# Performance work log

Measured on AMD Instinct MI355X. Metric: run time of the kernel, lower is better.

## Reference

```python
import jax, jax.numpy as jnp
import numpy as np


def _conv3x3(x, w, b):
    # stride 1, padding 1, NCHW / OIHW
    y = jax.lax.conv_general_dilated(x, w, (1, 1), ((1, 1), (1, 1)),
                                     dimension_numbers=('NCHW', 'OIHW', 'NCHW'))
    return y + b[None, :, None, None]


def _bilinear(img, py, px):
    """Bilinear sample img [B,C,H,W] at float positions py,px [B,H,W].
    Out-of-bounds corners contribute zero (zero padding), matching DCNv2."""
    B, C, H, W = img.shape
    y0f = jnp.floor(py)
    x0f = jnp.floor(px)
    wy = (py - y0f)[:, None]  # [B,1,H,W]
    wx = (px - x0f)[:, None]
    y0 = y0f.astype(jnp.int32)
    x0 = x0f.astype(jnp.int32)
    flat = img.reshape(B, C, H * W)

    def g(iy, ix):
        valid = ((iy >= 0) & (iy < H) & (ix >= 0) & (ix < W))
        lin = (jnp.clip(iy, 0, H - 1) * W + jnp.clip(ix, 0, W - 1)).reshape(B, 1, -1)
        idx = jnp.broadcast_to(lin, (B, C, lin.shape[-1]))
        v = jnp.take_along_axis(flat, idx, axis=2).reshape(B, C, *iy.shape[1:])
        return v * valid[:, None].astype(img.dtype)

    v00 = g(y0, x0)
    v01 = g(y0, x0 + 1)
    v10 = g(y0 + 1, x0)
    v11 = g(y0 + 1, x0 + 1)
    return (v00 * (1 - wy) * (1 - wx) + v01 * (1 - wy) * wx
            + v10 * wy * (1 - wx) + v11 * wy * wx)


def _dcn(x, ow, ob, w, b):
    """Modulated deformable conv (DCNv2), 3x3, stride 1, pad 1, dg=1."""
    B, C, H, W = x.shape
    om = _conv3x3(x, ow, ob)                       # [B,27,H,W]
    o1, o2, m = jnp.split(om, 3, axis=1)
    off = jnp.concatenate([o1, o2], axis=1)        # [B,18,H,W]
    mask = jax.nn.sigmoid(m)                       # [B,9,H,W]
    oy = off[:, 0::2]                              # [B,9,H,W] y-offset per tap
    ox = off[:, 1::2]                              # [B,9,H,W] x-offset per tap
    ys = jnp.arange(H, dtype=x.dtype)[None, :, None]
    xs = jnp.arange(W, dtype=x.dtype)[None, None, :]
    acc = jnp.zeros((B, w.shape[0], H, W), x.dtype)
    for k in range(9):  # fixed small kernel-tap loop
        ky, kx = divmod(k, 3)
        py = ys + (ky - 1) + oy[:, k]
        px = xs + (kx - 1) + ox[:, k]
        v = _bilinear(x, py, px) * mask[:, k][:, None]   # [B,C,H,W]
        acc = acc + jnp.einsum('bchw,oc->bohw', v, w[:, :, ky, kx])
    return acc + b[None, :, None, None]


def setup_inputs() -> dict:
    key = jax.random.key(0)
    ks = jax.random.split(key, 8)
    B, H, W = 4, 96, 96
    x = jax.random.normal(ks[0], (B, 64, H, W), jnp.float32)

    def offw(k, cin):
        return jax.random.normal(k, (27, cin, 3, 3), jnp.float32) * 0.01

    def mainw(k, cout, cin):
        return jax.random.normal(k, (cout, cin, 3, 3), jnp.float32) * (1.0 / np.sqrt(cin * 9))

    return {
        'x': x,
        'ow1': offw(ks[1], 64), 'ob1': jnp.zeros((27,), jnp.float32),
        'w1': mainw(ks[2], 64, 64), 'b1': jnp.zeros((64,), jnp.float32),
        'ow2': offw(ks[3], 64), 'ob2': jnp.zeros((27,), jnp.float32),
        'w2': mainw(ks[4], 512, 64), 'b2': jnp.zeros((512,), jnp.float32),
        'ow3': offw(ks[5], 512), 'ob3': jnp.zeros((27,), jnp.float32),
        'w3': mainw(ks[6], 256, 512), 'b3': jnp.zeros((256,), jnp.float32),
    }


def reference(x, ow1, ob1, w1, b1, ow2, ob2, w2, b2, ow3, ob3, w3, b3):
    y = _dcn(x, ow1, ob1, w1, b1)
    y = _dcn(y, ow2, ob2, w2, b2)
    y = _dcn(y, ow3, ob3, w3, b3)
    return y
```

## Files before the change

### kernel.cpp

```cpp
#include <hip/hip_runtime.h>
#include <stdint.h>


#define HH 96
#define WW 96
#define BBATCH 4
#define HWP (HH*WW)
#define PTOT (BBATCH*HWP)

typedef _Float16 f16x8 __attribute__((ext_vector_type(8)));
typedef _Float16 h2    __attribute__((ext_vector_type(2)));
typedef float f32x4 __attribute__((ext_vector_type(4)));

union U16x8 { uint4 q; _Float16 h[8]; h2 v[4]; };
union UB    { uint4 q; f16x8 f; };
union UH4   { uint2 d; _Float16 h[4]; };

__global__ void k_nchw2nhwc(const float* __restrict__ in, _Float16* __restrict__ out){
  __shared__ float t[32][33];
  int b = blockIdx.z;
  int p0 = blockIdx.x*32, c0 = blockIdx.y*32;
  int tx = threadIdx.x, ty = threadIdx.y;
  #pragma unroll
  for(int i=0;i<32;i+=8)
    t[ty+i][tx] = in[((size_t)(b*64 + c0+ty+i))*HWP + p0+tx];
  __syncthreads();
  #pragma unroll
  for(int i=0;i<32;i+=8)
    out[((size_t)(b*HWP + p0+ty+i))*64 + c0+tx] = (_Float16)t[tx][ty+i];
}

template<int CIN>
__global__ void k_tow(const float* __restrict__ ow, _Float16* __restrict__ owT){
  int i = blockIdx.x*256 + threadIdx.x;
  if(i >= 9*32*CIN) return;
  int c = i % CIN; int j = (i/CIN)&31; int k = i/(CIN*32);
  owT[i] = (j<27) ? (_Float16)ow[((size_t)(j*CIN + c))*9 + k] : (_Float16)0.f;
}

template<int CIN,int COUT>
__global__ void k_tw(const float* __restrict__ w, _Float16* __restrict__ wTf){
  int i = blockIdx.x*256 + threadIdx.x;
  if(i >= 9*COUT*CIN) return;
  int c = i % CIN; int o = (i/CIN)%COUT; int k = i/(CIN*COUT);
  int g = c>>5, quad = (c>>3)&3, j = c&7;
  int ob = o>>4, l15 = o&15;
  size_t dst = ((((size_t)k*(CIN/32) + g)*(COUT/16) + ob)*64 + quad*16 + l15)*8 + j;
  wTf[dst] = (_Float16)w[((size_t)(o*CIN + c))*9 + k];
}

template<int CIN,int NT>
__launch_bounds__(256,2)
__global__ void k_goffs(const _Float16* __restrict__ xin, const _Float16* __restrict__ owT,
                        float* __restrict__ om){
  __shared__ __align__(16) _Float16 As[64*40];
  __shared__ __align__(16) _Float16 Bs[32*40];
  int pos0 = blockIdx.x*64;
  int K0 = blockIdx.y*NT;
  float* omo = om + (size_t)blockIdx.y*PTOT*32;
  int t = threadIdx.x;
  int lane = t&63, wave = t>>6;
  int quad = lane>>4, l15 = lane&15;
  f32x4 acc[2] = {};
  int pa = t>>2, ca = (t&3)*8;
  int P = pos0 + pa;
  int b = P/HWP, rem = P%HWP;
  int y = rem/WW, x = rem%WW;
  #pragma unroll 1
  for(int k=K0;k<K0+NT;k++){
    int iy = y + k/3 - 1, ix = x + k%3 - 1;
    bool valid = (iy>=0)&&(iy<HH)&&(ix>=0)&&(ix<WW);
    const _Float16* src = xin + (((size_t)b*HWP + iy*WW + ix)*CIN) + ca;
    #pragma unroll 1
    for(int c0=0;c0<CIN;c0+=32){
      uint4 av = make_uint4(0,0,0,0);
      if(valid) av = *(const uint4*)(src + c0);
      *(uint4*)&As[pa*40 + ca] = av;
      if(t < 128){
        int j = t>>2;
        *(uint4*)&Bs[j*40 + ca] = *(const uint4*)(owT + ((size_t)k*32 + j)*CIN + c0 + ca);
      }
      __syncthreads();
      UB afu; afu.q = *(const uint4*)&As[(wave*16 + l15)*40 + quad*8];
      #pragma unroll
      for(int ni=0;ni<2;ni++){
        UB bu; bu.q = *(const uint4*)&Bs[(ni*16 + l15)*40 + quad*8];
        acc[ni] = __builtin_amdgcn_mfma_f32_16x16x32_f16(afu.f, bu.f, acc[ni], 0,0,0);
      }
      __syncthreads();
    }
  }
  #pragma unroll
  for(int ni=0;ni<2;ni++)
    #pragma unroll
    for(int r=0;r<4;r++){
      int row = wave*16 + quad*4 + r;
      omo[(size_t)(pos0+row)*32 + ni*16 + l15] = acc[ni][r];
    }
}

template<int NS>
__global__ void k_prep(const float* __restrict__ om, const float* __restrict__ ob,
                       float* __restrict__ pym){
  int i = blockIdx.x*256 + threadIdx.x;
  if(i >= PTOT*9) return;
  int k = i%9, p = i/9;
  int rem = p%HWP;
  int y = rem/WW, x = rem%WW;
  float oy=0.f, ox=0.f, mm=0.f;
  #pragma unroll
  for(int s=0;s<NS;s++){
    const float* o = om + (size_t)s*PTOT*32 + (size_t)p*32;
    oy += o[2*k]; ox += o[2*k+1]; mm += o[18+k];
  }
  oy += ob[2*k]; ox += ob[2*k+1]; mm += ob[18+k];
  float m = 1.f/(1.f + expf(-mm));
  pym[(size_t)i*3+0] = (float)(y + k/3 - 1) + oy;
  pym[(size_t)i*3+1] = (float)(x + k%3 - 1) + ox;
  pym[(size_t)i*3+2] = m;
}

template<int CIN,int COUT,int BN,int MODE>
__launch_bounds__(256,2)
__global__ void k_gmain(const _Float16* __restrict__ xin, const float* __restrict__ pym,
                        const _Float16* __restrict__ wTf, const float* __restrict__ bias,
                        void* __restrict__ outv){
  constexpr int NW = BN/4;
  constexpr int NF = NW/16;
  constexpr int KG = CIN/32;
  constexpr int OB = COUT/16;
  constexpr int SPT = CIN/64;
  constexpr int NZ = (MODE==1) ? 3 : 1;
  constexpr int KN = (MODE==1) ? 3 : 9;
  constexpr int S = KN*SPT;
  __shared__ __align__(16) _Float16 As[2][64*72];
  int bx = blockIdx.x;
  int q = bx>>3, r = bx&7;
  int z = q - (q/NZ)*NZ;
  int lin = r*((gridDim.x>>3)/NZ) + q/NZ;
  int pos0 = lin*64;
  int o0 = blockIdx.y*BN;
  int K0 = (MODE==1) ? z*3 : 0;
  int t = threadIdx.x;
  int lane = t&63, wave = t>>6;
  int quad = lane>>4, l15 = lane&15;
  f32x4 acc[4][NF] = {};
  int pa = t>>2, ca = (t&3)*16;
  int P = pos0 + pa;
  int b = P/HWP;
  const _Float16* base = xin + (size_t)b*HWP*CIN + ca;
  const uint4* wf = (const uint4*)wTf;
  int obBase = (o0>>4) + wave*NF;

  h2 Wc[4]; int oc_[4];
  h2 Wn[4]; int ocn[4];
  int kc = K0;

  auto tapParams = [&](int k, h2* W, int* oc){
    const float* pp = pym + ((size_t)P*9 + k)*3;
    float py = pp[0], px = pp[1], mk = pp[2];
    float y0f = floorf(py), x0f = floorf(px);
    float wy = py - y0f, wx = px - x0f;
    int iy0 = (int)y0f, ix0 = (int)x0f;
    int iy1 = iy0+1, ix1 = ix0+1;
    bool vy0 = (iy0>=0)&&(iy0<HH), vy1 = (iy1>=0)&&(iy1<HH);
    bool vx0 = (ix0>=0)&&(ix0<WW), vx1 = (ix1>=0)&&(ix1<WW);
    float w00 = (vy0&&vx0) ? (1.f-wy)*(1.f-wx)*mk : 0.f;
    float w01 = (vy0&&vx1) ? (1.f-wy)*wx*mk      : 0.f;
    float w10 = (vy1&&vx0) ? wy*(1.f-wx)*mk      : 0.f;
    float w11 = (vy1&&vx1) ? wy*wx*mk            : 0.f;
    int cy0 = min(max(iy0,0),HH-1), cy1 = min(max(iy1,0),HH-1);
    int cx0 = min(max(ix0,0),WW-1), cx1 = min(max(ix1,0),WW-1);
    W[0] = h2{(_Float16)w00,(_Float16)w00};
    W[1] = h2{(_Float16)w01,(_Float16)w01};
    W[2] = h2{(_Float16)w10,(_Float16)w10};
    W[3] = h2{(_Float16)w11,(_Float16)w11};
    oc[0] = (cy0*WW+cx0)*CIN;
    oc[1] = (cy0*WW+cx1)*CIN;
    oc[2] = (cy1*WW+cx0)*CIN;
    oc[3] = (cy1*WW+cx1)*CIN;
  };

  uint4 Bq[2][NF];
  const uint4* wB = wf + (size_t)(K0*KG)*OB*64 + lane;

  tapParams(K0, Wc, oc_);
  {
    U16x8 nc[4][2];
    #pragma unroll
    for(int c=0;c<4;c++){
      const _Float16* pp = base + oc_[c];
      nc[c][0].q = *(const uint4*)(pp);
      nc[c][1].q = *(const uint4*)(pp + 8);
    }
    #pragma unroll
    for(int ks=0;ks<2;ks++)
      #pragma unroll
      for(int ni=0;ni<NF;ni++)
        Bq[ks][ni] = wB[(size_t)ks*OB*64 + (size_t)(obBase+ni)*64];
    wB += 2*OB*64;
    U16x8 rr0, rr1;
    #pragma unroll
    for(int j=0;j<4;j++){
      rr0.v[j] = nc[0][0].v[j]*Wc[0] + nc[1][0].v[j]*Wc[1] + nc[2][0].v[j]*Wc[2] + nc[3][0].v[j]*Wc[3];
      rr1.v[j] = nc[0][1].v[j]*Wc[0] + nc[1][1].v[j]*Wc[1] + nc[2][1].v[j]*Wc[2] + nc[3][1].v[j]*Wc[3];
    }
    *(uint4*)&As[0][pa*72 + ca]     = rr0.q;
    *(uint4*)&As[0][pa*72 + ca + 8] = rr1.q;
  }
  if constexpr (SPT==1){
    if(S>1) tapParams(K0+1, Wn, ocn);
  }

  int buf = 0;
  #pragma unroll 1
  for(int s=0;s<S;s++){
    __syncthreads();
    U16x8 nc[4][2];
    bool more = (s+1 < S);
    if(more){
      if constexpr (SPT==1){
        #pragma unroll
        for(int c=0;c<4;c++){ Wc[c]=Wn[c]; oc_[c]=ocn[c]; }
      } else {
        int tn = K0 + (s+1)/SPT;
        if(tn != kc){
          kc = tn;
          tapParams(tn, Wc, oc_);
        }
      }
      int c0 = ((s+1)%SPT)*64;
      #pragma unroll
      for(int c=0;c<4;c++){
        const _Float16* pp = base + oc_[c] + c0;
        nc[c][0].q = *(const uint4*)(pp);
        nc[c][1].q = *(const uint4*)(pp + 8);
      }
    }
    UB afu[2][4];
    #pragma unroll
    for(int ks=0;ks<2;ks++)
      #pragma unroll
      for(int mi=0;mi<4;mi++)
        afu[ks][mi].q = *(const uint4*)&As[buf][(mi*16 + l15)*72 + ks*32 + quad*8];
    #pragma unroll
    for(int ks=0;ks<2;ks++)
      #pragma unroll
      for(int ni=0;ni<NF;ni++){
        UB bu; bu.q = Bq[ks][ni];
        #pragma unroll
        for(int mi=0;mi<4;mi++)
          acc[mi][ni] = __builtin_amdgcn_mfma_f32_16x16x32_f16(afu[ks][mi].f, bu.f, acc[mi][ni], 0,0,0);
      }
    if(more){
      #pragma unroll
      for(int ks=0;ks<2;ks++)
        #pragma unroll
        for(int ni=0;ni<NF;ni++)
          Bq[ks][ni] = wB[(size_t)ks*OB*64 + (size_t)(obBase+ni)*64];
      wB += 2*OB*64;
      if constexpr (SPT==1){
        if(s+2 < S) tapParams(K0+s+2, Wn, ocn);
      }
      U16x8 rr0, rr1;
      #pragma unroll
      for(int j=0;j<4;j++){
        rr0.v[j] = nc[0][0].v[j]*Wc[0] + nc[1][0].v[j]*Wc[1] + nc[2][0].v[j]*Wc[2] + nc[3][0].v[j]*Wc[3];
        rr1.v[j] = nc[0][1].v[j]*Wc[0] + nc[1][1].v[j]*Wc[1] + nc[2][1].v[j]*Wc[2] + nc[3][1].v[j]*Wc[3];
      }
      *(uint4*)&As[buf^1][pa*72 + ca]     = rr0.q;
      *(uint4*)&As[buf^1][pa*72 + ca + 8] = rr1.q;
    }
    buf ^= 1;
  }

  #pragma unroll
  for(int mi=0;mi<4;mi++){
    #pragma unroll
    for(int ni=0;ni<NF;ni++){
      int col = o0 + wave*NW + ni*16 + l15;
      if(MODE==1){
        float* out = (float*)outv + (size_t)z*PTOT*COUT;
        #pragma unroll
        for(int r=0;r<4;r++){
          int row = pos0 + mi*16 + quad*4 + r;
          out[(size_t)row*COUT + col] = acc[mi][ni][r];
        }
      } else {
        float bo = bias[col];
        _Float16* out = (_Float16*)outv;
        #pragma unroll
        for(int r=0;r<4;r++){
          int row = pos0 + mi*16 + quad*4 + r;
          out[(size_t)row*COUT + col] = (_Float16)(acc[mi][ni][r]+bo);
        }
      }
    }
  }
}

template<int COUT>
__global__ void k_redA(const float* __restrict__ part, const float* __restrict__ bias,
                       _Float16* __restrict__ out){
  int i4 = blockIdx.x*256 + threadIdx.x;
  constexpr int N4 = PTOT*COUT/4;
  if(i4 >= N4) return;
  const float4* p = (const float4*)part;
  float4 a = p[i4], b = p[i4 + N4], c = p[i4 + 2*N4];
  int col0 = (i4*4) & (COUT-1);
  float4 bi = *(const float4*)(bias + col0);
  UH4 r;
  r.h[0] = (_Float16)(a.x+b.x+c.x+bi.x);
  r.h[1] = (_Float16)(a.y+b.y+c.y+bi.y);
  r.h[2] = (_Float16)(a.z+b.z+c.z+bi.z);
  r.h[3] = (_Float16)(a.w+b.w+c.w+bi.w);
  *(uint2*)(out + (size_t)i4*4) = r.d;
}

__global__ void k_redT(const float* __restrict__ part, const float* __restrict__ bias,
                       float* __restrict__ out){
  __shared__ float t[32][33];
  constexpr int COUT = 256;
  constexpr size_t SL = (size_t)PTOT*COUT;
  int b = blockIdx.z;
  int p0 = blockIdx.x*32, c0 = blockIdx.y*32;
  int tx = threadIdx.x, ty = threadIdx.y;
  #pragma unroll
  for(int i=0;i<32;i+=8){
    size_t idx = ((size_t)(b*HWP + p0+ty+i))*COUT + c0+tx;
    t[ty+i][tx] = part[idx] + part[idx+SL] + part[idx+2*SL];
  }
  __syncthreads();
  #pragma unroll
  for(int i=0;i<32;i+=8)
    out[((size_t)(b*COUT + c0+ty+i))*HWP + p0+tx] = t[tx][ty+i] + bias[c0+ty+i];
}

extern "C" void kernel_launch(void* const* d_in, const int* in_sizes, int n_in,
                              void* d_out, int out_size, void* d_ws, size_t ws_size,
                              hipStream_t stream){
  (void)in_sizes; (void)n_in; (void)out_size;
  const float* x   = (const float*)d_in[0];
  const float* ow1 = (const float*)d_in[1];
  const float* ob1 = (const float*)d_in[2];
  const float* w1  = (const float*)d_in[3];
  const float* b1  = (const float*)d_in[4];
  const float* ow2 = (const float*)d_in[5];
  const float* ob2 = (const float*)d_in[6];
  const float* w2  = (const float*)d_in[7];
  const float* b2  = (const float*)d_in[8];
  const float* ow3 = (const float*)d_in[9];
  const float* ob3 = (const float*)d_in[10];
  const float* w3  = (const float*)d_in[11];
  const float* b3  = (const float*)d_in[12];

  char* p = (char*)d_ws;
  auto carve = [&](size_t bytes)->char*{ char* r = p; p += (bytes + 255) & ~(size_t)255; return r; };
  _Float16* xh  = (_Float16*)carve((size_t)PTOT*64*2);
  _Float16* y1  = (_Float16*)carve((size_t)PTOT*64*2);
  _Float16* y2  = (_Float16*)carve((size_t)PTOT*512*2);
  _Float16* owT = (_Float16*)carve((size_t)9*32*512*2);
  _Float16* wT  = (_Float16*)carve((size_t)9*512*512*2);
  float*    om  = (float*)carve((size_t)3*PTOT*32*4);
  float*    pym = (float*)carve((size_t)PTOT*9*3*4);
  bool splitK = ws_size >= ((size_t)p - (size_t)d_ws) + (size_t)3*PTOT*256*4 + 4096;
  float* part = splitK ? (float*)carve((size_t)3*PTOT*256*4) : nullptr;

  k_nchw2nhwc<<<dim3(288,2,BBATCH), dim3(32,8), 0, stream>>>(x, xh);

  if(splitK){
    k_tow<64><<<(9*32*64+255)/256,256,0,stream>>>(ow1, owT);
    k_tw<64,64><<<(9*64*64+255)/256,256,0,stream>>>(w1, wT);
    k_goffs<64,3><<<dim3(PTOT/64,3),256,0,stream>>>(xh, owT, om);
    k_prep<3><<<(PTOT*9+255)/256,256,0,stream>>>(om, ob1, pym);
    k_gmain<64,64,64,1><<<dim3(3*PTOT/64,1,1),256,0,stream>>>(xh, pym, wT, b1, part);
    k_redA<64><<<(PTOT*64/4+255)/256,256,0,stream>>>(part, b1, y1);

    k_tow<64><<<(9*32*64+255)/256,256,0,stream>>>(ow2, owT);
    k_tw<64,512><<<(9*512*64+255)/256,256,0,stream>>>(w2, wT);
    k_goffs<64,3><<<dim3(PTOT/64,3),256,0,stream>>>(y1, owT, om);
    k_prep<3><<<(PTOT*9+255)/256,256,0,stream>>>(om, ob2, pym);
    k_gmain<64,512,256,0><<<dim3(PTOT/64,2),256,0,stream>>>(y1, pym, wT, b2, y2);

    k_tow<512><<<(9*32*512+255)/256,256,0,stream>>>(ow3, owT);
    k_tw<512,256><<<(9*256*512+255)/256,256,0,stream>>>(w3, wT);
    k_goffs<512,3><<<dim3(PTOT/64,3),256,0,stream>>>(y2, owT, om);
    k_prep<3><<<(PTOT*9+255)/256,256,0,stream>>>(om, ob3, pym);
    k_gmain<512,256,256,1><<<dim3(3*PTOT/64,1,1),256,0,stream>>>(y2, pym, wT, b3, part);
    k_redT<<<dim3(288,8,4),dim3(32,8),0,stream>>>(part, b3, (float*)d_out);
  } else {
    k_tow<64><<<(9*32*64+255)/256,256,0,stream>>>(ow1, owT);
    k_tw<64,64><<<(9*64*64+255)/256,256,0,stream>>>(w1, wT);
    k_goffs<64,9><<<dim3(PTOT/64,1),256,0,stream>>>(xh, owT, om);
    k_prep<1><<<(PTOT*9+255)/256,256,0,stream>>>(om, ob1, pym);
    k_gmain<64,64,64,0><<<dim3(PTOT/64,1),256,0,stream>>>(xh, pym, wT, b1, y1);

    k_tow<64><<<(9*32*64+255)/256,256,0,stream>>>(ow2, owT);
    k_tw<64,512><<<(9*512*64+255)/256,256,0,stream>>>(w2, wT);
    k_goffs<64,9><<<dim3(PTOT/64,1),256,0,stream>>>(y1, owT, om);
    k_prep<1><<<(PTOT*9+255)/256,256,0,stream>>>(om, ob2, pym);
    k_gmain<64,512,256,0><<<dim3(PTOT/64,2),256,0,stream>>>(y1, pym, wT, b2, y2);

    k_tow<512><<<(9*32*512+255)/256,256,0,stream>>>(ow3, owT);
    k_tw<512,256><<<(9*256*512+255)/256,256,0,stream>>>(w3, wT);
    k_goffs<512,9><<<dim3(PTOT/64,1),256,0,stream>>>(y2, owT, om);
    k_prep<1><<<(PTOT*9+255)/256,256,0,stream>>>(om, ob3, pym);
    k_gmain<512,256,256,0><<<dim3(PTOT/64,1),256,0,stream>>>(y2, pym, wT, b3, y1);
    {
      struct L { static __global__ void tr(const _Float16* in, float* out){
        int i = blockIdx.x*256 + threadIdx.x;
        if(i >= PTOT*256) return;
        int c = i & 255, pnt = i >> 8;
        int bb = pnt / HWP, pr = pnt % HWP;
        out[((size_t)bb*256 + c)*HWP + pr] = (float)in[i];
      }};
      hipLaunchKernelGGL(L::tr, dim3((PTOT*256+255)/256), dim3(256), 0, stream,
                         (const _Float16*)y1, (float*)d_out);
    }
  }
}
```

Baseline: 403.2 us.

## Prefetch gathered neighbour rows two stages ahead in multi-chunk deformable GEMM

For the SPT>1 path (input channels split into several 64-wide chunks per tap), the bilinear-gather global loads are issued two pipeline stages ahead using ping-pong register buffers, with the loop manually unrolled by two. Tap parameters for the next tap are computed early and held in a separate set of registers. This hides gather latency behind more MFMA work but increases register pressure, and the unroll-by-two assumes S is even.

```diff
diff --git a/kernel.cpp b/kernel.cpp
--- a/kernel.cpp
+++ b/kernel.cpp
@@ -152,10 +152,6 @@
   const uint4* wf = (const uint4*)wTf;
   int obBase = (o0>>4) + wave*NF;
 
-  h2 Wc[4]; int oc_[4];
-  h2 Wn[4]; int ocn[4];
-  int kc = K0;
-
   auto tapParams = [&](int k, h2* W, int* oc){
     const float* pp = pym + ((size_t)P*9 + k)*3;
     float py = pp[0], px = pp[1], mk = pp[2];
@@ -183,95 +179,187 @@
 
   uint4 Bq[2][NF];
   const uint4* wB = wf + (size_t)(K0*KG)*OB*64 + lane;
-
-  tapParams(K0, Wc, oc_);
-  {
-    U16x8 nc[4][2];
-    #pragma unroll
-    for(int c=0;c<4;c++){
-      const _Float16* pp = base + oc_[c];
-      nc[c][0].q = *(const uint4*)(pp);
-      nc[c][1].q = *(const uint4*)(pp + 8);
-    }
-    #pragma unroll
-    for(int ks=0;ks<2;ks++)
-      #pragma unroll
-      for(int ni=0;ni<NF;ni++)
-        Bq[ks][ni] = wB[(size_t)ks*OB*64 + (size_t)(obBase+ni)*64];
-    wB += 2*OB*64;
-    U16x8 rr0, rr1;
-    #pragma unroll
-    for(int j=0;j<4;j++){
-      rr0.v[j] = nc[0][0].v[j]*Wc[0] + nc[1][0].v[j]*Wc[1] + nc[2][0].v[j]*Wc[2] + nc[3][0].v[j]*Wc[3];
-      rr1.v[j] = nc[0][1].v[j]*Wc[0] + nc[1][1].v[j]*Wc[1] + nc[2][1].v[j]*Wc[2] + nc[3][1].v[j]*Wc[3];
-    }
-    *(uint4*)&As[0][pa*72 + ca]     = rr0.q;
-    *(uint4*)&As[0][pa*72 + ca + 8] = rr1.q;
-  }
-  if constexpr (SPT==1){
-    if(S>1) tapParams(K0+1, Wn, ocn);
-  }
-
   int buf = 0;
-  #pragma unroll 1
-  for(int s=0;s<S;s++){
-    __syncthreads();
-    U16x8 nc[4][2];
-    bool more = (s+1 < S);
-    if(more){
-      if constexpr (SPT==1){
-        #pragma unroll
-        for(int c=0;c<4;c++){ Wc[c]=Wn[c]; oc_[c]=ocn[c]; }
-      } else {
-        int tn = K0 + (s+1)/SPT;
-        if(tn != kc){
-          kc = tn;
-          tapParams(tn, Wc, oc_);
-        }
-      }
-      int c0 = ((s+1)%SPT)*64;
+
+  if constexpr (SPT > 1){
+    h2 Wcur[4], Wnxt[4];
+    int ocCur[4], ocNxt[4];
+    tapParams(K0, Wcur, ocCur);
+    U16x8 ncA[4][2], ncB[4][2];
+    {
+      U16x8 c0v[4][2];
       #pragma unroll
       for(int c=0;c<4;c++){
-        const _Float16* pp = base + oc_[c] + c0;
-        nc[c][0].q = *(const uint4*)(pp);
-        nc[c][1].q = *(const uint4*)(pp + 8);
-      }
-    }
-    UB afu[2][4];
-    #pragma unroll
-    for(int ks=0;ks<2;ks++)
-      #pragma unroll
-      for(int mi=0;mi<4;mi++)
-        afu[ks][mi].q = *(const uint4*)&As[buf][(mi*16 + l15)*72 + ks*32 + quad*8];
-    #pragma unroll
-    for(int ks=0;ks<2;ks++)
-      #pragma unroll
-      for(int ni=0;ni<NF;ni++){
-        UB bu; bu.q = Bq[ks][ni];
-        #pragma unroll
-        for(int mi=0;mi<4;mi++)
-          acc[mi][ni] = __builtin_amdgcn_mfma_f32_16x16x32_f16(afu[ks][mi].f, bu.f, acc[mi][ni], 0,0,0);
-      }
-    if(more){
+        const _Float16* pp = base + ocCur[c];
+        c0v[c][0].q = *(const uint4*)(pp);
+        c0v[c][1].q = *(const uint4*)(pp + 8);
+      }
       #pragma unroll
       for(int ks=0;ks<2;ks++)
         #pragma unroll
         for(int ni=0;ni<NF;ni++)
           Bq[ks][ni] = wB[(size_t)ks*OB*64 + (size_t)(obBase+ni)*64];
       wB += 2*OB*64;
-      if constexpr (SPT==1){
-        if(s+2 < S) tapParams(K0+s+2, Wn, ocn);
-      }
+      U16x8 rr0, rr1;
+      #pragma unroll
+      for(int j=0;j<4;j++){
+        rr0.v[j] = c0v[0][0].v[j]*Wcur[0] + c0v[1][0].v[j]*Wcur[1] + c0v[2][0].v[j]*Wcur[2] + c0v[3][0].v[j]*Wcur[3];
+        rr1.v[j] = c0v[0][1].v[j]*Wcur[0] + c0v[1][1].v[j]*Wcur[1] + c0v[2][1].v[j]*Wcur[2] + c0v[3][1].v[j]*Wcur[3];
+      }
+      *(uint4*)&As[0][pa*72 + ca]     = rr0.q;
+      *(uint4*)&As[0][pa*72 + ca + 8] = rr1.q;
+      #pragma unroll
+      for(int c=0;c<4;c++){
+        const _Float16* pp = base + ocCur[c] + 64;
+        ncA[c][0].q = *(const uint4*)(pp);
+        ncA[c][1].q = *(const uint4*)(pp + 8);
+      }
+    }
+
+    auto stage = [&](int s, U16x8 (&ncC)[4][2], U16x8 (&ncN)[4][2]){
+      __syncthreads();
+      bool more  = (s+1 < S);
+      bool more2 = (s+2 < S);
+      if(s > 0 && (s % SPT) == 0){
+        #pragma unroll
+        for(int j=0;j<4;j++){ Wcur[j]=Wnxt[j]; ocCur[j]=ocNxt[j]; }
+      }
+      if(more2){
+        int sm2 = (s+2) % SPT;
+        if(sm2 == 0) tapParams(K0 + (s+2)/SPT, Wnxt, ocNxt);
+        bool useNxt = (sm2 < 2);
+        int ocS[4];
+        #pragma unroll
+        for(int c=0;c<4;c++) ocS[c] = useNxt ? ocNxt[c] : ocCur[c];
+        int c0 = sm2*64;
+        #pragma unroll
+        for(int c=0;c<4;c++){
+          const _Float16* pp = base + ocS[c] + c0;
+          ncN[c][0].q = *(const uint4*)(pp);
+          ncN[c][1].q = *(const uint4*)(pp + 8);
+        }
+      }
+      UB afu[2][4];
+      #pragma unroll
+      for(int ks=0;ks<2;ks++)
+        #pragma unroll
+        for(int mi=0;mi<4;mi++)
+          afu[ks][mi].q = *(const uint4*)&As[buf][(mi*16 + l15)*72 + ks*32 + quad*8];
+      #pragma unroll
+      for(int ks=0;ks<2;ks++)
+        #pragma unroll
+        for(int ni=0;ni<NF;ni++){
+          UB bu; bu.q = Bq[ks][ni];
+          #pragma unroll
+          for(int mi=0;mi<4;mi++)
+            acc[mi][ni] = __builtin_amdgcn_mfma_f32_16x16x32_f16(afu[ks][mi].f, bu.f, acc[mi][ni], 0,0,0);
+        }
+      if(more){
+        #pragma unroll
+        for(int ks=0;ks<2;ks++)
+          #pragma unroll
+          for(int ni=0;ni<NF;ni++)
+            Bq[ks][ni] = wB[(size_t)ks*OB*64 + (size_t)(obBase+ni)*64];
+        wB += 2*OB*64;
+        bool lerpNxt = (((s+1) % SPT) == 0);
+        h2 Wl[4];
+        #pragma unroll
+        for(int j=0;j<4;j++) Wl[j] = lerpNxt ? Wnxt[j] : Wcur[j];
+        U16x8 rr0, rr1;
+        #pragma unroll
+        for(int j=0;j<4;j++){
+          rr0.v[j] = ncC[0][0].v[j]*Wl[0] + ncC[1][0].v[j]*Wl[1] + ncC[2][0].v[j]*Wl[2] + ncC[3][0].v[j]*Wl[3];
+          rr1.v[j] = ncC[0][1].v[j]*Wl[0] + ncC[1][1].v[j]*Wl[1] + ncC[2][1].v[j]*Wl[2] + ncC[3][1].v[j]*Wl[3];
+        }
+        *(uint4*)&As[buf^1][pa*72 + ca]     = rr0.q;
+        *(uint4*)&As[buf^1][pa*72 + ca + 8] = rr1.q;
+      }
+      buf ^= 1;
+    };
+
+    #pragma unroll 1
+    for(int ss=0; ss<S; ss+=2){
+      stage(ss,   ncA, ncB);
+      stage(ss+1, ncB, ncA);
+    }
+  } else {
+    h2 Wc[4]; int oc_[4];
+    h2 Wn[4]; int ocn[4];
+    tapParams(K0, Wc, oc_);
+    {
+      U16x8 nc[4][2];
+      #pragma unroll
+      for(int c=0;c<4;c++){
+        const _Float16* pp = base + oc_[c];
+        nc[c][0].q = *(const uint4*)(pp);
+        nc[c][1].q = *(const uint4*)(pp + 8);
+      }
+      #pragma unroll
+      for(int ks=0;ks<2;ks++)
+        #pragma unroll
+        for(int ni=0;ni<NF;ni++)
+          Bq[ks][ni] = wB[(size_t)ks*OB*64 + (size_t)(obBase+ni)*64];
+      wB += 2*OB*64;
       U16x8 rr0, rr1;
       #pragma unroll
       for(int j=0;j<4;j++){
         rr0.v[j] = nc[0][0].v[j]*Wc[0] + nc[1][0].v[j]*Wc[1] + nc[2][0].v[j]*Wc[2] + nc[3][0].v[j]*Wc[3];
         rr1.v[j] = nc[0][1].v[j]*Wc[0] + nc[1][1].v[j]*Wc[1] + nc[2][1].v[j]*Wc[2] + nc[3][1].v[j]*Wc[3];
       }
-      *(uint4*)&As[buf^1][pa*72 + ca]     = rr0.q;
-      *(uint4*)&As[buf^1][pa*72 + ca + 8] = rr1.q;
-    }
-    buf ^= 1;
+      *(uint4*)&As[0][pa*72 + ca]     = rr0.q;
+      *(uint4*)&As[0][pa*72 + ca + 8] = rr1.q;
+    }
+    if(S>1) tapParams(K0+1, Wn, ocn);
+
+    #pragma unroll 1
+    for(int s=0;s<S;s++){
+      __syncthreads();
+      U16x8 nc[4][2];
+      bool more = (s+1 < S);
+      if(more){
+        #pragma unroll
+        for(int c=0;c<4;c++){ Wc[c]=Wn[c]; oc_[c]=ocn[c]; }
+        #pragma unroll
+        for(int c=0;c<4;c++){
+          const _Float16* pp = base + oc_[c];
+          nc[c][0].q = *(const uint4*)(pp);
+          nc[c][1].q = *(const uint4*)(pp + 8);
+        }
+      }
+      UB afu[2][4];
+      #pragma unroll
+      for(int ks=0;ks<2;ks++)
+        #pragma unroll
+        for(int mi=0;mi<4;mi++)
+          afu[ks][mi].q = *(const uint4*)&As[buf][(mi*16 + l15)*72 + ks*32 + quad*8];
+      #pragma unroll
+      for(int ks=0;ks<2;ks++)
+        #pragma unroll
+        for(int ni=0;ni<NF;ni++){
+          UB bu; bu.q = Bq[ks][ni];
+          #pragma unroll
+          for(int mi=0;mi<4;mi++)
+            acc[mi][ni] = __builtin_amdgcn_mfma_f32_16x16x32_f16(afu[ks][mi].f, bu.f, acc[mi][ni], 0,0,0);
+        }
+      if(more){
+        #pragma unroll
+        for(int ks=0;ks<2;ks++)
+          #pragma unroll
+          for(int ni=0;ni<NF;ni++)
+            Bq[ks][ni] = wB[(size_t)ks*OB*64 + (size_t)(obBase+ni)*64];
+        wB += 2*OB*64;
+        if(s+2 < S) tapParams(K0+s+2, Wn, ocn);
+        U16x8 rr0, rr1;
+        #pragma unroll
+        for(int j=0;j<4;j++){
+          rr0.v[j] = nc[0][0].v[j]*Wc[0] + nc[1][0].v[j]*Wc[1] + nc[2][0].v[j]*Wc[2] + nc[3][0].v[j]*Wc[3];
+          rr1.v[j] = nc[0][1].v[j]*Wc[0] + nc[1][1].v[j]*Wc[1] + nc[2][1].v[j]*Wc[2] + nc[3][1].v[j]*Wc[3];
+        }
+        *(uint4*)&As[buf^1][pa*72 + ca]     = rr0.q;
+        *(uint4*)&As[buf^1][pa*72 + ca + 8] = rr1.q;
+      }
+      buf ^= 1;
+    }
   }
 
   #pragma unroll
```

New measurement: 400.3 us. No clear change (-0.7%).

## Parameterize gather-GEMM M tile and deepen corner prefetch for wide-CIN layers

Applied to the files above, without the earlier changes.

Adds a BM template parameter so the deformable gather-GEMM can use 32-row position tiles, which doubles grid size for the 512-channel layers and spreads the gather across more blocks. For CIN>1 slices, corner loads are issued two stages ahead using alternating register buffers, so bilinear gather latency overlaps with more MFMA work. This costs more registers for the extra corner buffers and halves the M reuse of each B fragment, so weight loads grow relative to compute.

```diff
diff --git a/kernel.cpp b/kernel.cpp
--- a/kernel.cpp
+++ b/kernel.cpp
@@ -120,41 +120,41 @@
   pym[(size_t)i*3+2] = m;
 }
 
-template<int CIN,int COUT,int BN,int MODE>
+template<int CIN,int COUT,int BM,int BN,int MODE>
 __launch_bounds__(256,2)
 __global__ void k_gmain(const _Float16* __restrict__ xin, const float* __restrict__ pym,
                         const _Float16* __restrict__ wTf, const float* __restrict__ bias,
                         void* __restrict__ outv){
   constexpr int NW = BN/4;
   constexpr int NF = NW/16;
+  constexpr int MI = BM/16;
   constexpr int KG = CIN/32;
   constexpr int OB = COUT/16;
   constexpr int SPT = CIN/64;
   constexpr int NZ = (MODE==1) ? 3 : 1;
   constexpr int KN = (MODE==1) ? 3 : 9;
   constexpr int S = KN*SPT;
-  __shared__ __align__(16) _Float16 As[2][64*72];
+  constexpr int TPR = 256/BM;
+  constexpr int CPT = 64/TPR;
+  constexpr int NU  = CPT/8;
+  __shared__ __align__(16) _Float16 As[2][BM*72];
   int bx = blockIdx.x;
   int q = bx>>3, r = bx&7;
   int z = q - (q/NZ)*NZ;
   int lin = r*((gridDim.x>>3)/NZ) + q/NZ;
-  int pos0 = lin*64;
+  int pos0 = lin*BM;
   int o0 = blockIdx.y*BN;
   int K0 = (MODE==1) ? z*3 : 0;
   int t = threadIdx.x;
   int lane = t&63, wave = t>>6;
   int quad = lane>>4, l15 = lane&15;
-  f32x4 acc[4][NF] = {};
-  int pa = t>>2, ca = (t&3)*16;
+  f32x4 acc[MI][NF] = {};
+  int pa = t/TPR, ca = (t%TPR)*CPT;
   int P = pos0 + pa;
   int b = P/HWP;
   const _Float16* base = xin + (size_t)b*HWP*CIN + ca;
   const uint4* wf = (const uint4*)wTf;
   int obBase = (o0>>4) + wave*NF;
-
-  h2 Wc[4]; int oc_[4];
-  h2 Wn[4]; int ocn[4];
-  int kc = K0;
 
   auto tapParams = [&](int k, h2* W, int* oc){
     const float* pp = pym + ((size_t)P*9 + k)*3;
@@ -181,101 +181,137 @@
     oc[3] = (cy1*WW+cx1)*CIN;
   };
 
+  auto lerpWrite = [&](U16x8 (&nc)[4][NU], h2* W, int dbuf){
+    #pragma unroll
+    for(int u=0;u<NU;u++){
+      U16x8 rr;
+      #pragma unroll
+      for(int j=0;j<4;j++)
+        rr.v[j] = nc[0][u].v[j]*W[0] + nc[1][u].v[j]*W[1] + nc[2][u].v[j]*W[2] + nc[3][u].v[j]*W[3];
+      *(uint4*)&As[dbuf][pa*72 + ca + u*8] = rr.q;
+    }
+  };
+  auto loadCorners = [&](U16x8 (&nc)[4][NU], const int* oc, int c0){
+    #pragma unroll
+    for(int c=0;c<4;c++){
+      const _Float16* pp = base + oc[c] + c0;
+      #pragma unroll
+      for(int u=0;u<NU;u++)
+        nc[c][u].q = *(const uint4*)(pp + u*8);
+    }
+  };
+
   uint4 Bq[2][NF];
   const uint4* wB = wf + (size_t)(K0*KG)*OB*64 + lane;
-
-  tapParams(K0, Wc, oc_);
-  {
-    U16x8 nc[4][2];
-    #pragma unroll
-    for(int c=0;c<4;c++){
-      const _Float16* pp = base + oc_[c];
-      nc[c][0].q = *(const uint4*)(pp);
-      nc[c][1].q = *(const uint4*)(pp + 8);
-    }
+  auto loadB = [&](){
     #pragma unroll
     for(int ks=0;ks<2;ks++)
       #pragma unroll
       for(int ni=0;ni<NF;ni++)
         Bq[ks][ni] = wB[(size_t)ks*OB*64 + (size_t)(obBase+ni)*64];
     wB += 2*OB*64;
-    U16x8 rr0, rr1;
-    #pragma unroll
-    for(int j=0;j<4;j++){
-      rr0.v[j] = nc[0][0].v[j]*Wc[0] + nc[1][0].v[j]*Wc[1] + nc[2][0].v[j]*Wc[2] + nc[3][0].v[j]*Wc[3];
-      rr1.v[j] = nc[0][1].v[j]*Wc[0] + nc[1][1].v[j]*Wc[1] + nc[2][1].v[j]*Wc[2] + nc[3][1].v[j]*Wc[3];
-    }
-    *(uint4*)&As[0][pa*72 + ca]     = rr0.q;
-    *(uint4*)&As[0][pa*72 + ca + 8] = rr1.q;
-  }
-  if constexpr (SPT==1){
-    if(S>1) tapParams(K0+1, Wn, ocn);
-  }
-
-  int buf = 0;
-  #pragma unroll 1
-  for(int s=0;s<S;s++){
-    __syncthreads();
-    U16x8 nc[4][2];
-    bool more = (s+1 < S);
-    if(more){
-      if constexpr (SPT==1){
-        #pragma unroll
-        for(int c=0;c<4;c++){ Wc[c]=Wn[c]; oc_[c]=ocn[c]; }
-      } else {
-        int tn = K0 + (s+1)/SPT;
-        if(tn != kc){
-          kc = tn;
-          tapParams(tn, Wc, oc_);
-        }
-      }
-      int c0 = ((s+1)%SPT)*64;
-      #pragma unroll
-      for(int c=0;c<4;c++){
-        const _Float16* pp = base + oc_[c] + c0;
-        nc[c][0].q = *(const uint4*)(pp);
-        nc[c][1].q = *(const uint4*)(pp + 8);
-      }
-    }
-    UB afu[2][4];
+  };
+  auto doMFMA = [&](int dbuf){
+    UB afu[2][MI];
     #pragma unroll
     for(int ks=0;ks<2;ks++)
       #pragma unroll
-      for(int mi=0;mi<4;mi++)
-        afu[ks][mi].q = *(const uint4*)&As[buf][(mi*16 + l15)*72 + ks*32 + quad*8];
+      for(int mi=0;mi<MI;mi++)
+        afu[ks][mi].q = *(const uint4*)&As[dbuf][(mi*16 + l15)*72 + ks*32 + quad*8];
     #pragma unroll
     for(int ks=0;ks<2;ks++)
       #pragma unroll
       for(int ni=0;ni<NF;ni++){
         UB bu; bu.q = Bq[ks][ni];
         #pragma unroll
-        for(int mi=0;mi<4;mi++)
+        for(int mi=0;mi<MI;mi++)
           acc[mi][ni] = __builtin_amdgcn_mfma_f32_16x16x32_f16(afu[ks][mi].f, bu.f, acc[mi][ni], 0,0,0);
       }
-    if(more){
-      #pragma unroll
-      for(int ks=0;ks<2;ks++)
-        #pragma unroll
-        for(int ni=0;ni<NF;ni++)
-          Bq[ks][ni] = wB[(size_t)ks*OB*64 + (size_t)(obBase+ni)*64];
-      wB += 2*OB*64;
-      if constexpr (SPT==1){
+  };
+
+  int buf = 0;
+
+  if constexpr (SPT > 1){
+    h2 Wcur[4], Wnxt[4];
+    int ocCur[4], ocNxt[4];
+    tapParams(K0, Wcur, ocCur);
+    U16x8 ncA[4][NU], ncB[4][NU];
+    {
+      U16x8 c0v[4][NU];
+      loadCorners(c0v, ocCur, 0);
+      loadB();
+      lerpWrite(c0v, Wcur, 0);
+      loadCorners(ncA, ocCur, 64);
+    }
+
+    auto stage = [&](int s, U16x8 (&ncC)[4][NU], U16x8 (&ncN)[4][NU]){
+      __syncthreads();
+      bool more  = (s+1 < S);
+      bool more2 = (s+2 < S);
+      if(s > 0 && (s % SPT) == 0){
+        #pragma unroll
+        for(int j=0;j<4;j++){ Wcur[j]=Wnxt[j]; ocCur[j]=ocNxt[j]; }
+      }
+      if(more2){
+        int sm2 = (s+2) % SPT;
+        if(sm2 == 0) tapParams(K0 + (s+2)/SPT, Wnxt, ocNxt);
+        bool useNxt = (sm2 < 2);
+        int ocS[4];
+        #pragma unroll
+        for(int c=0;c<4;c++) ocS[c] = useNxt ? ocNxt[c] : ocCur[c];
+        loadCorners(ncN, ocS, sm2*64);
+      }
+      doMFMA(buf);
+      if(more){
+        loadB();
+        bool lerpNxt = (((s+1) % SPT) == 0);
+        h2 Wl[4];
+        #pragma unroll
+        for(int j=0;j<4;j++) Wl[j] = lerpNxt ? Wnxt[j] : Wcur[j];
+        lerpWrite(ncC, Wl, buf^1);
+      }
+      buf ^= 1;
+    };
+
+    #pragma unroll 1
+    for(int ss=0; ss<S; ss+=2){
+      stage(ss,   ncA, ncB);
+      stage(ss+1, ncB, ncA);
+    }
+  } else {
+    h2 Wc[4]; int oc_[4];
+    h2 Wn[4]; int ocn[4];
+    tapParams(K0, Wc, oc_);
+    {
+      U16x8 nc[4][NU];
+      loadCorners(nc, oc_, 0);
+      loadB();
+      lerpWrite(nc, Wc, 0);
+    }
+    if(S>1) tapParams(K0+1, Wn, ocn);
+
+    #pragma unroll 1
+    for(int s=0;s<S;s++){
+      __syncthreads();
+      U16x8 nc[4][NU];
+      bool more = (s+1 < S);
+      if(more){
+        #pragma unroll
+        for(int c=0;c<4;c++){ Wc[c]=Wn[c]; oc_[c]=ocn[c]; }
+        loadCorners(nc, oc_, 0);
+      }
+      doMFMA(buf);
+      if(more){
+        loadB();
         if(s+2 < S) tapParams(K0+s+2, Wn, ocn);
-      }
-      U16x8 rr0, rr1;
-      #pragma unroll
-      for(int j=0;j<4;j++){
-        rr0.v[j] = nc[0][0].v[j]*Wc[0] + nc[1][0].v[j]*Wc[1] + nc[2][0].v[j]*Wc[2] + nc[3][0].v[j]*Wc[3];
-        rr1.v[j] = nc[0][1].v[j]*Wc[0] + nc[1][1].v[j]*Wc[1] + nc[2][1].v[j]*Wc[2] + nc[3][1].v[j]*Wc[3];
-      }
-      *(uint4*)&As[buf^1][pa*72 + ca]     = rr0.q;
-      *(uint4*)&As[buf^1][pa*72 + ca + 8] = rr1.q;
-    }
-    buf ^= 1;
-  }
-
-  #pragma unroll
-  for(int mi=0;mi<4;mi++){
+        lerpWrite(nc, Wc, buf^1);
+      }
+      buf ^= 1;
+    }
+  }
+
+  #pragma unroll
+  for(int mi=0;mi<MI;mi++){
     #pragma unroll
     for(int ni=0;ni<NF;ni++){
       int col = o0 + wave*NW + ni*16 + l15;
@@ -373,39 +409,39 @@
     k_tw<64,64><<<(9*64*64+255)/256,256,0,stream>>>(w1, wT);
     k_goffs<64,3><<<dim3(PTOT/64,3),256,0,stream>>>(xh, owT, om);
     k_prep<3><<<(PTOT*9+255)/256,256,0,stream>>>(om, ob1, pym);
-    k_gmain<64,64,64,1><<<dim3(3*PTOT/64,1,1),256,0,stream>>>(xh, pym, wT, b1, part);
+    k_gmain<64,64,64,64,1><<<dim3(3*PTOT/64,1,1),256,0,stream>>>(xh, pym, wT, b1, part);
     k_redA<64><<<(PTOT*64/4+255)/256,256,0,stream>>>(part, b1, y1);
 
     k_tow<64><<<(9*32*64+255)/256,256,0,stream>>>(ow2, owT);
     k_tw<64,512><<<(9*512*64+255)/256,256,0,stream>>>(w2, wT);
     k_goffs<64,3><<<dim3(PTOT/64,3),256,0,stream>>>(y1, owT, om);
     k_prep<3><<<(PTOT*9+255)/256,256,0,stream>>>(om, ob2, pym);
-    k_gmain<64,512,256,0><<<dim3(PTOT/64,2),256,0,stream>>>(y1, pym, wT, b2, y2);
+    k_gmain<64,512,32,256,0><<<dim3(PTOT/32,2),256,0,stream>>>(y1, pym, wT, b2, y2);
 
     k_tow<512><<<(9*32*512+255)/256,256,0,stream>>>(ow3, owT);
     k_tw<512,256><<<(9*256*512+255)/256,256,0,stream>>>(w3, wT);
     k_goffs<512,3><<<dim3(PTOT/64,3),256,0,stream>>>(y2, owT, om);
     k_prep<3><<<(PTOT*9+255)/256,256,0,stream>>>(om, ob3, pym);
-    k_gmain<512,256,256,1><<<dim3(3*PTOT/64,1,1),256,0,stream>>>(y2, pym, wT, b3, part);
+    k_gmain<512,256,32,256,1><<<dim3(3*PTOT/32,1,1),256,0,stream>>>(y2, pym, wT, b3, part);
     k_redT<<<dim3(288,8,4),dim3(32,8),0,stream>>>(part, b3, (float*)d_out);
   } else {
     k_tow<64><<<(9*32*64+255)/256,256,0,stream>>>(ow1, owT);
     k_tw<64,64><<<(9*64*64+255)/256,256,0,stream>>>(w1, wT);
     k_goffs<64,9><<<dim3(PTOT/64,1),256,0,stream>>>(xh, owT, om);
     k_prep<1><<<(PTOT*9+255)/256,256,0,stream>>>(om, ob1, pym);
-    k_gmain<64,64,64,0><<<dim3(PTOT/64,1),256,0,stream>>>(xh, pym, wT, b1, y1);
+    k_gmain<64,64,64,64,0><<<dim3(PTOT/64,1),256,0,stream>>>(xh, pym, wT, b1, y1);
 
     k_tow<64><<<(9*32*64+255)/256,256,0,stream>>>(ow2, owT);
     k_tw<64,512><<<(9*512*64+255)/256,256,0,stream>>>(w2, wT);
     k_goffs<64,9><<<dim3(PTOT/64,1),256,0,stream>>>(y1, owT, om);
     k_prep<1><<<(PTOT*9+255)/256,256,0,stream>>>(om, ob2, pym);
-    k_gmain<64,512,256,0><<<dim3(PTOT/64,2),256,0,stream>>>(y1, pym, wT, b2, y2);
+    k_gmain<64,512,32,256,0><<<dim3(PTOT/32,2),256,0,stream>>>(y1, pym, wT, b2, y2);
 
     k_tow<512><<<(9*32*512+255)/256,256,0,stream>>>(ow3, owT);
     k_tw<512,256><<<(9*256*512+255)/256,256,0,stream>>>(w3, wT);
     k_goffs<512,9><<<dim3(PTOT/64,1),256,0,stream>>>(y2, owT, om);
     k_prep<1><<<(PTOT*9+255)/256,256,0,stream>>>(om, ob3, pym);
-    k_gmain<512,256,256,0><<<dim3(PTOT/64,1),256,0,stream>>>(y2, pym, wT, b3, y1);
+    k_gmain<512,256,32,256,0><<<dim3(PTOT/32,1),256,0,stream>>>(y2, pym, wT, b3, y1);
     {
       struct L { static __global__ void tr(const _Float16* in, float* out){
         int i = blockIdx.x*256 + threadIdx.x;
```

Measured after the change: 435.3 us. +7.9%, slower.
